# Performance work log

Measured on AMD Instinct MI355X. Metric: run time of the kernel, lower is better.

The kernel has to match this reference:

```python
import jax, jax.numpy as jnp
import numpy as np
from jax import lax

EPS = 1e-6            # cfg.positive
GAUSS_DIM = (32, 32)  # cfg.iou_gauss_dim
TOP_K_CONF = 100      # cfg.nms_top_k_conf
TOP_K_IOU = 20        # cfg.nms_top_k_iou


def unnormal_gaussian(mask_shape, loc):
    # loc: [B, N, 4] = (cx, cy, w, h) in normalized [0,1] coords.
    # Unnormalized anisotropic gaussian rendered on an HxW grid.
    H, W = mask_shape
    cx, cy, w, h = loc[..., 0], loc[..., 1], loc[..., 2], loc[..., 3]
    ys = (jnp.arange(H, dtype=loc.dtype) + 0.5) / H
    xs = (jnp.arange(W, dtype=loc.dtype) + 0.5) / W
    dx = (xs[None, None, None, :] - cx[..., None, None]) / (w[..., None, None] + 1e-4)
    dy = (ys[None, None, :, None] - cy[..., None, None]) / (h[..., None, None] + 1e-4)
    return jnp.exp(-0.5 * (dx * dx + dy * dy))  # [B, N, H, W]


def _take2(t, idx):
    # twoIndexThree: t [B,N,D], idx [B,K] -> [B,K,D]
    return jnp.take_along_axis(t, idx[..., None], axis=1)


def detect(conf, loc, mask):
    # conf: [B,P] object scores; loc: [B,P,4]; mask: [B,P,Dm]
    sorted_conf, idx = lax.top_k(conf, TOP_K_CONF)
    sorted_loc = _take2(loc, idx)
    sorted_mask = _take2(mask, idx)
    g = unnormal_gaussian(GAUSS_DIM, sorted_loc)  # [B,N,Hg,Wg]
    # pairwise gaussian IoU: sum(min) / sum(max); use min+max == a+b identity
    inter = jnp.sum(jnp.minimum(g[:, :, None], g[:, None, :]), axis=(-2, -1))  # [B,N,N]
    s = jnp.sum(g, axis=(-2, -1))
    union = s[:, :, None] + s[:, None, :] - inter
    iou = inter / union
    iou_max = jnp.max(jnp.triu(iou, 1), axis=1)   # max overlap with any earlier (higher-conf) box
    _, keep = lax.top_k(-iou_max, TOP_K_IOU)      # keep K least-overlapping boxes
    return iou, sorted_loc, sorted_mask, sorted_conf, keep


def ae_scaled_loss(original, iou, keep, loc, conf):
    conf_matrix = conf[:, :, None] * conf[:, None, :]   # outer product [B,N,N]
    final_scale = iou * jnp.triu(conf_matrix, 1)
    kept_loc = _take2(loc, keep)                        # [B,K,4]
    # surrogate AutoEncoder per-box loss (AutoEncoder class not in source)
    ae_loss = jnp.mean(kept_loc ** 2, axis=-1)          # [B,K]
    B, N = final_scale.shape[0], final_scale.shape[1]
    K = keep.shape[1]
    ae_grid = jnp.zeros_like(final_scale).at[jnp.arange(B)[:, None], keep].set(
        jnp.broadcast_to(ae_loss[..., None], (B, K, N)))
    return jnp.mean(ae_grid * final_scale)


def variance_loss(original, loc, mask, conf, proto):
    B, C, H, W = original.shape
    Hp, Wp = proto.shape[1], proto.shape[2]
    ug = unnormal_gaussian((Hp, Wp), loc)                           # [B,K,Hp,Wp]
    assembled = jax.nn.sigmoid(jnp.einsum('bhwp,bkp->bkhw', proto, mask))  # lincomb
    attention = assembled * ug
    mc = attention * conf[:, :, None, None]                         # maskConfidence
    denom = jnp.sum(mc, axis=1, keepdims=True) + EPS
    final_conf = 1.0 - jnp.sum(mc * mc / denom, axis=1)             # [B,Hp,Wp]
    final_conf = jnp.where(jnp.isnan(final_conf), 0.0, final_conf)
    # bilinear, align_corners=False == jax linear resize (half-pixel centers)
    resized = jax.image.resize(final_conf[:, None], (B, 1, H, W), method='linear')[:, 0]
    total = jnp.sum(resized, axis=0)                                 # [H,W]
    wmean = jnp.einsum('bchw,bhw->chw', original, resized) / total
    sq = (original - wmean) ** 2
    wvar = sq * resized[:, None] / (total + EPS)
    return jnp.sum(wvar) / Hp * B


def reference(original, loc, conf, mask, proto):
    conf_p = jax.nn.softmax(conf, axis=2)[:, :, 1]
    iou, s_loc, s_mask, s_conf, keep = detect(conf_p, loc, mask)
    ae = ae_scaled_loss(original, iou, keep, s_loc, s_conf)
    k_loc = _take2(s_loc, keep)
    k_mask = _take2(s_mask, keep)
    k_conf = jnp.take_along_axis(s_conf, keep, axis=1)
    var = variance_loss(original, k_loc, k_mask, k_conf, proto)
    return jnp.stack([var, ae])  # [variance_loss, ae_loss]


def setup_inputs() -> dict:
    key = jax.random.key(0)
    k1, k2, k3, k4, k5, k6 = jax.random.split(key, 6)
    B, P, Dm = 2, 19248, 32
    H = W = 550
    Hp = Wp = 138
    original = jax.random.normal(k1, (B, 3, H, W), dtype=jnp.float32)
    centers = jax.random.uniform(k2, (B, P, 2), dtype=jnp.float32)
    sizes = jax.random.uniform(k3, (B, P, 2), dtype=jnp.float32, minval=0.1, maxval=0.5)
    loc = jnp.concatenate([centers, sizes], axis=-1)                 # (cx,cy,w,h)
    conf = jax.random.normal(k4, (B, P, 2), dtype=jnp.float32)
    mask = jax.random.normal(k5, (B, P, Dm), dtype=jnp.float32) * 0.2
    proto = jax.random.normal(k6, (B, Hp, Wp, Dm), dtype=jnp.float32) * 0.5
    return {"original": original, "loc": loc, "conf": conf, "mask": mask, "proto": proto}
```

## Files before the change

kernel.cpp:

```cpp
#include <hip/hip_runtime.h>
#include <hip/hip_bf16.h>
#include <math.h>

constexpr int B   = 2;
constexpr int P   = 19248;
constexpr int N   = 100;
constexpr int K   = 20;
constexpr int GD  = 32;
constexpr int GP  = GD * GD;
constexpr int HP  = 138;
constexpr int HPP = HP * HP;
constexpr int H   = 550;
constexpr int W   = 550;
constexpr int DM  = 32;
constexpr float EPS = 1e-6f;
constexpr int NBIN = 2048;
constexpr int CAND = 2048;
constexpr int NPAIR = N * (N - 1) / 2;

constexpr int OFS_IDX   = 0;
constexpr int OFS_SCONF = OFS_IDX   + B * N;
constexpr int OFS_SLOC  = OFS_SCONF + B * N;
constexpr int OFS_IOU   = OFS_SLOC  + B * N * 4;
constexpr int OFS_KLOC  = OFS_IOU   + B * N * N;
constexpr int OFS_KMASK = OFS_KLOC  + B * K * 4;
constexpr int OFS_KCONF = OFS_KMASK + B * K * DM;
constexpr int OFS_FC    = OFS_KCONF + B * K;

__global__ __launch_bounds__(1024) void k_topk(
    const float* __restrict__ conf, const float* __restrict__ loc,
    float* __restrict__ wsf, int* __restrict__ wsi, float* __restrict__ out) {
  const int b = blockIdx.x;
  const int t = threadIdx.x;
  constexpr int EPT = (P + 1023) / 1024;
  if (b == 0 && t < 2) out[t] = 0.0f;

  __shared__ int   hist[NBIN];
  __shared__ int   s_T, s_cnt;
  __shared__ float cv[CAND];
  __shared__ int   ci[CAND];
  __shared__ float outv[N];
  __shared__ int   outi[N];

  for (int q = t; q < NBIN; q += 1024) hist[q] = 0;
  if (t == 0) s_cnt = 0;
  __syncthreads();

  float v[EPT];
#pragma unroll
  for (int j = 0; j < EPT; j++) {
    int p = j * 1024 + t;
    if (p < P) {
      float c0 = conf[(b * P + p) * 2 + 0];
      float c1 = conf[(b * P + p) * 2 + 1];
      float m  = fmaxf(c0, c1);
      float e0 = expf(c0 - m), e1 = expf(c1 - m);
      v[j] = e1 / (e0 + e1);
      atomicAdd(&hist[__float_as_uint(v[j]) >> 19], 1);
    } else {
      v[j] = -1.0f;
    }
  }
  __syncthreads();

  if (t == 0) {
    int acc = 0, bin = NBIN - 1;
    for (; bin >= 0; bin--) { acc += hist[bin]; if (acc >= N) break; }
    s_T = bin;
  }
  __syncthreads();
  const int T = s_T;

#pragma unroll
  for (int j = 0; j < EPT; j++) {
    int p = j * 1024 + t;
    if (p < P && (int)(__float_as_uint(v[j]) >> 19) >= T) {
      int pos = atomicAdd(&s_cnt, 1);
      if (pos < CAND) { cv[pos] = v[j]; ci[pos] = p; }
    }
  }
  __syncthreads();
  const int M = min(s_cnt, CAND);

#pragma unroll
  for (int q = 0; q < CAND / 1024; q++) {
    int c = t + q * 1024;
    if (c < M) {
      float mv = cv[c]; int mi = ci[c];
      int rank = 0;
      for (int j = 0; j < M; j++) {
        float jv = cv[j]; int ji = ci[j];
        rank += (jv > mv || (jv == mv && ji < mi)) ? 1 : 0;
      }
      if (rank < N) { outv[rank] = mv; outi[rank] = mi; }
    }
  }
  __syncthreads();

  if (t < N) {
    wsi[OFS_IDX + b * N + t]   = outi[t];
    wsf[OFS_SCONF + b * N + t] = outv[t];
  }
  if (t < N * 4) {
    int k = t >> 2, d = t & 3;
    wsf[OFS_SLOC + (b * N + k) * 4 + d] = loc[(b * P + outi[k]) * 4 + d];
  }
}

__global__ __launch_bounds__(256) void k_iou(float* __restrict__ wsf) {
  const int blk = blockIdx.x;
  const int b = blk / NPAIR;
  const int r = blk - b * NPAIR;
  int i = (int)((199.0f - sqrtf((float)(39601 - 8 * r))) * 0.5f);
  i = min(max(i, 0), N - 2);
  while (i < N - 2 && ((i + 1) * (2 * N - 2 - i)) / 2 <= r) i++;
  while (i > 0 && (i * (2 * N - 1 - i)) / 2 > r) i--;
  const int j = i + 1 + (r - (i * (2 * N - 1 - i)) / 2);

  const int t = threadIdx.x;
  const float* li = &wsf[OFS_SLOC + (b * N + i) * 4];
  const float* lj = &wsf[OFS_SLOC + (b * N + j) * 4];
  const float cxi = li[0], cyi = li[1], wi = li[2], hi = li[3];
  const float cxj = lj[0], cyj = lj[1], wj = lj[2], hj = lj[3];

  float smin = 0.0f, ssi = 0.0f, ssj = 0.0f;
#pragma unroll
  for (int q = 0; q < 4; q++) {
    int pix = t + q * 256;
    int y = pix >> 5, x = pix & 31;
    float xs = (x + 0.5f) / 32.0f, ys = (y + 0.5f) / 32.0f;
    float dxi = (xs - cxi) / (wi + 1e-4f);
    float dyi = (ys - cyi) / (hi + 1e-4f);
    float gi = expf(-0.5f * (dxi * dxi + dyi * dyi));
    float dxj = (xs - cxj) / (wj + 1e-4f);
    float dyj = (ys - cyj) / (hj + 1e-4f);
    float gj = expf(-0.5f * (dxj * dxj + dyj * dyj));
    smin += fminf(gi, gj);
    ssi += gi;
    ssj += gj;
  }
  for (int off = 32; off > 0; off >>= 1) {
    smin += __shfl_down(smin, off);
    ssi  += __shfl_down(ssi, off);
    ssj  += __shfl_down(ssj, off);
  }
  __shared__ float sp[3][4];
  if ((t & 63) == 0) {
    int w4 = t >> 6;
    sp[0][w4] = smin; sp[1][w4] = ssi; sp[2][w4] = ssj;
  }
  __syncthreads();
  if (t == 0) {
    float inter = sp[0][0] + sp[0][1] + sp[0][2] + sp[0][3];
    float si    = sp[1][0] + sp[1][1] + sp[1][2] + sp[1][3];
    float sj    = sp[2][0] + sp[2][1] + sp[2][2] + sp[2][3];
    wsf[OFS_IOU + (b * N + i) * N + j] = inter / (si + sj - inter);
  }
}

__global__ __launch_bounds__(1024) void k_select(
    const float* __restrict__ mask, float* __restrict__ wsf,
    int* __restrict__ wsi, float* __restrict__ out) {
  const int b = blockIdx.x;
  const int t = threadIdx.x;
  __shared__ float siou[N * N];
  __shared__ float sconf[N];
  __shared__ unsigned int mbits[N];
  __shared__ int   keep[K];
  __shared__ float coef[K];
  __shared__ float red[16];

  for (int idx = t; idx < N * N; idx += 1024) {
    int row = idx / N, col = idx - row * N;
    siou[idx] = (col > row) ? wsf[OFS_IOU + b * N * N + idx] : 0.0f;
  }
  if (t < N) { sconf[t] = wsf[OFS_SCONF + b * N + t]; mbits[t] = 0u; }
  __syncthreads();

  for (int idx = t; idx < N * N; idx += 1024) {
    int col = idx % N;
    atomicMax(&mbits[col], __float_as_uint(siou[idx]));
  }
  __syncthreads();

  if (t < N) {
    unsigned int vb = mbits[t];
    int rank = 0;
    for (int j = 0; j < N; j++) {
      unsigned int jb = mbits[j];
      rank += (jb < vb || (jb == vb && j < t)) ? 1 : 0;
    }
    if (rank < K) keep[rank] = t;
  }
  __syncthreads();

  if (t < K) {
    int r = keep[t];
    float c = sconf[r];
    wsf[OFS_KCONF + b * K + t] = c;
    const float* kl = &wsf[OFS_SLOC + (b * N + r) * 4];
    float ael = 0.25f * (kl[0] * kl[0] + kl[1] * kl[1] + kl[2] * kl[2] + kl[3] * kl[3]);
    coef[t] = ael * c;
  }
  if (t < K * 4) {
    int k = t >> 2, d = t & 3;
    wsf[OFS_KLOC + (b * K + k) * 4 + d] = wsf[OFS_SLOC + (b * N + keep[k]) * 4 + d];
  }
  if (t < K * DM) {
    int k = t >> 5, d = t & 31;
    int orig = wsi[OFS_IDX + b * N + keep[k]];
    wsf[OFS_KMASK + (b * K + k) * DM + d] = mask[(b * P + orig) * DM + d];
  }
  __syncthreads();

  float acc = 0.0f;
  for (int kc = t; kc < K * N; kc += 1024) {
    int k = kc / N, c = kc - k * N;
    int r = keep[k];
    if (c > r) acc += siou[r * N + c] * sconf[c] * coef[k];
  }
  for (int off = 32; off > 0; off >>= 1) acc += __shfl_down(acc, off);
  if ((t & 63) == 0) red[t >> 6] = acc;
  __syncthreads();
  if (t == 0) {
    float s = 0.0f;
    for (int w2 = 0; w2 < 16; w2++) s += red[w2];
    atomicAdd(out + 1, s * (1.0f / (float)(B * N * N)));
  }
}

__global__ __launch_bounds__(256) void k_fc(
    const float* __restrict__ proto, float* __restrict__ wsf) {
  const int b = blockIdx.y;
  const int t = threadIdx.x;
  const int pix = blockIdx.x * 256 + t;
  __shared__ float kl[K * 4];
  __shared__ float kc[K];
  __shared__ float km[K * DM];
  for (int q = t; q < K * 4; q += 256) kl[q] = wsf[OFS_KLOC + b * K * 4 + q];
  for (int q = t; q < K; q += 256) kc[q] = wsf[OFS_KCONF + b * K + q];
  for (int q = t; q < K * DM; q += 256) km[q] = wsf[OFS_KMASK + b * K * DM + q];
  __syncthreads();
  if (pix >= HPP) return;
  const int h = pix / HP, w2 = pix - h * HP;

  float pv[DM];
  const float4* pp = (const float4*)&proto[(size_t)(b * HPP + pix) * DM];
#pragma unroll
  for (int q = 0; q < DM / 4; q++) {
    float4 f = pp[q];
    pv[q * 4 + 0] = f.x; pv[q * 4 + 1] = f.y;
    pv[q * 4 + 2] = f.z; pv[q * 4 + 3] = f.w;
  }
  const float ysv = (h + 0.5f) / 138.0f;
  const float xsv = (w2 + 0.5f) / 138.0f;
  float sum1 = 0.0f, sum2 = 0.0f;
#pragma unroll
  for (int k = 0; k < K; k++) {
    float dot = 0.0f;
#pragma unroll
    for (int d = 0; d < DM; d++) dot += pv[d] * km[k * DM + d];
    float a  = 1.0f / (1.0f + expf(-dot));
    float dx = (xsv - kl[k * 4 + 0]) / (kl[k * 4 + 2] + 1e-4f);
    float dy = (ysv - kl[k * 4 + 1]) / (kl[k * 4 + 3] + 1e-4f);
    float ug = expf(-0.5f * (dx * dx + dy * dy));
    float att = a * ug * kc[k];
    sum1 += att;
    sum2 += att * att;
  }
  float fc = 1.0f - sum2 / (sum1 + EPS);
  if (fc != fc) fc = 0.0f;
  wsf[OFS_FC + b * HPP + pix] = fc;
}

__global__ __launch_bounds__(256) void k_var(
    const float* __restrict__ orig, const float* __restrict__ wsf,
    float* __restrict__ out) {
  const int t = threadIdx.x;
  float acc = 0.0f;
  for (int pix = blockIdx.x * 256 + t; pix < H * W; pix += 256 * 256) {
    const int h = pix / W, w2 = pix - h * W;
    const float sc = 138.0f / 550.0f;
    float sy = (h + 0.5f) * sc - 0.5f;
    float sx = (w2 + 0.5f) * sc - 0.5f;
    float fy0 = floorf(sy), fx0 = floorf(sx);
    float wy = sy - fy0, wx = sx - fx0;
    int y0 = max(0, (int)fy0), y1 = min(HP - 1, (int)fy0 + 1);
    int x0 = max(0, (int)fx0), x1 = min(HP - 1, (int)fx0 + 1);
    float r0, r1;
    {
      const float* fc = &wsf[OFS_FC + 0 * HPP];
      float v00 = fc[y0 * HP + x0], v01 = fc[y0 * HP + x1];
      float v10 = fc[y1 * HP + x0], v11 = fc[y1 * HP + x1];
      float top = v00 + (v01 - v00) * wx;
      float bot = v10 + (v11 - v10) * wx;
      r0 = top + (bot - top) * wy;
    }
    {
      const float* fc = &wsf[OFS_FC + 1 * HPP];
      float v00 = fc[y0 * HP + x0], v01 = fc[y0 * HP + x1];
      float v10 = fc[y1 * HP + x0], v11 = fc[y1 * HP + x1];
      float top = v00 + (v01 - v00) * wx;
      float bot = v10 + (v11 - v10) * wx;
      r1 = top + (bot - top) * wy;
    }
    float total = r0 + r1;
    float inv_t = 1.0f / total;
    float inv_te = 1.0f / (total + EPS);
#pragma unroll
    for (int c = 0; c < 3; c++) {
      float o0 = orig[((0 * 3 + c) * H + h) * W + w2];
      float o1 = orig[((1 * 3 + c) * H + h) * W + w2];
      float wm = (o0 * r0 + o1 * r1) * inv_t;
      float d0 = o0 - wm, d1 = o1 - wm;
      acc += (d0 * d0 * r0 + d1 * d1 * r1) * inv_te;
    }
  }
  for (int off = 32; off > 0; off >>= 1) acc += __shfl_down(acc, off);
  __shared__ float sp[4];
  if ((t & 63) == 0) sp[t >> 6] = acc;
  __syncthreads();
  if (t == 0)
    atomicAdd(out + 0, (sp[0] + sp[1] + sp[2] + sp[3]) * ((float)B / (float)HP));
}

extern "C" void kernel_launch(void* const* d_in, const int* in_sizes, int n_in,
                              void* d_out, int out_size, void* d_ws,
                              size_t ws_size, hipStream_t stream) {
  (void)in_sizes; (void)n_in; (void)out_size; (void)ws_size;
  const float* original = (const float*)d_in[0];
  const float* loc      = (const float*)d_in[1];
  const float* conf     = (const float*)d_in[2];
  const float* mask     = (const float*)d_in[3];
  const float* proto    = (const float*)d_in[4];
  float* out = (float*)d_out;
  float* wsf = (float*)d_ws;
  int*   wsi = (int*)d_ws;

  k_topk<<<B, 1024, 0, stream>>>(conf, loc, wsf, wsi, out);
  k_iou<<<B * NPAIR, 256, 0, stream>>>(wsf);
  k_select<<<B, 1024, 0, stream>>>(mask, wsf, wsi, out);
  k_fc<<<dim3((HPP + 255) / 256, B), 256, 0, stream>>>(proto, wsf);
  k_var<<<256, 256, 0, stream>>>(original, wsf, out);
}
```

Before: 134.6 us.

## Fuse all stages into one persistent kernel with software grid barriers

Merges the five kernels (top-k, pairwise IoU, keep-selection, proto attention map and variance) into one persistent 256-block kernel, separated by atomic-counter grid barriers, so launch gaps disappear. The IoU stage now uses one wavefront per pair instead of one 256-thread block per pair. The fc map is computed per output tile into shared memory and read there for the bilinear upsample, so no global fc buffer is needed. In exchange it recomputes fc at overlapping tile halos, and it depends on all 256 blocks of 1024 threads being resident at once, or the spin barriers deadlock.

```diff
diff --git a/kernel.cpp b/kernel.cpp
--- a/kernel.cpp
+++ b/kernel.cpp
@@ -6,8 +6,6 @@
 constexpr int P   = 19248;
 constexpr int N   = 100;
 constexpr int K   = 20;
-constexpr int GD  = 32;
-constexpr int GP  = GD * GD;
 constexpr int HP  = 138;
 constexpr int HPP = HP * HP;
 constexpr int H   = 550;
@@ -17,6 +15,9 @@
 constexpr int NBIN = 2048;
 constexpr int CAND = 2048;
 constexpr int NPAIR = N * (N - 1) / 2;
+constexpr int GRID = 256;
+constexpr int TS = 32;
+constexpr int TG = (W + TS - 1) / TS;
 
 constexpr int OFS_IDX   = 0;
 constexpr int OFS_SCONF = OFS_IDX   + B * N;
@@ -25,303 +26,317 @@
 constexpr int OFS_KLOC  = OFS_IOU   + B * N * N;
 constexpr int OFS_KMASK = OFS_KLOC  + B * K * 4;
 constexpr int OFS_KCONF = OFS_KMASK + B * K * DM;
-constexpr int OFS_FC    = OFS_KCONF + B * K;
-
-__global__ __launch_bounds__(1024) void k_topk(
-    const float* __restrict__ conf, const float* __restrict__ loc,
-    float* __restrict__ wsf, int* __restrict__ wsi, float* __restrict__ out) {
-  const int b = blockIdx.x;
+constexpr int OFS_BAR   = OFS_KCONF + B * K;
+
+__device__ __forceinline__ void grid_barrier(unsigned int* cnt) {
+  __syncthreads();
+  if (threadIdx.x == 0) {
+    __threadfence();
+    atomicAdd(cnt, 1u);
+    while (atomicAdd(cnt, 0u) < (unsigned)GRID) { }
+    __threadfence();
+  }
+  __syncthreads();
+}
+
+__global__ __launch_bounds__(1024) void k_fused(
+    const float* __restrict__ original, const float* __restrict__ loc,
+    const float* __restrict__ conf, const float* __restrict__ mask,
+    const float* __restrict__ proto, float* __restrict__ wsf,
+    int* __restrict__ wsi, unsigned int* __restrict__ bar,
+    float* __restrict__ out) {
+  const int blk = blockIdx.x;
   const int t = threadIdx.x;
-  constexpr int EPT = (P + 1023) / 1024;
-  if (b == 0 && t < 2) out[t] = 0.0f;
-
-  __shared__ int   hist[NBIN];
-  __shared__ int   s_T, s_cnt;
-  __shared__ float cv[CAND];
-  __shared__ int   ci[CAND];
+
+  __shared__ float smem[N * N];
   __shared__ float outv[N];
   __shared__ int   outi[N];
-
-  for (int q = t; q < NBIN; q += 1024) hist[q] = 0;
-  if (t == 0) s_cnt = 0;
-  __syncthreads();
-
-  float v[EPT];
-#pragma unroll
-  for (int j = 0; j < EPT; j++) {
-    int p = j * 1024 + t;
-    if (p < P) {
-      float c0 = conf[(b * P + p) * 2 + 0];
-      float c1 = conf[(b * P + p) * 2 + 1];
-      float m  = fmaxf(c0, c1);
-      float e0 = expf(c0 - m), e1 = expf(c1 - m);
-      v[j] = e1 / (e0 + e1);
-      atomicAdd(&hist[__float_as_uint(v[j]) >> 19], 1);
-    } else {
-      v[j] = -1.0f;
-    }
-  }
-  __syncthreads();
-
-  if (t == 0) {
-    int acc = 0, bin = NBIN - 1;
-    for (; bin >= 0; bin--) { acc += hist[bin]; if (acc >= N) break; }
-    s_T = bin;
-  }
-  __syncthreads();
-  const int T = s_T;
-
-#pragma unroll
-  for (int j = 0; j < EPT; j++) {
-    int p = j * 1024 + t;
-    if (p < P && (int)(__float_as_uint(v[j]) >> 19) >= T) {
-      int pos = atomicAdd(&s_cnt, 1);
-      if (pos < CAND) { cv[pos] = v[j]; ci[pos] = p; }
-    }
-  }
-  __syncthreads();
-  const int M = min(s_cnt, CAND);
-
-#pragma unroll
-  for (int q = 0; q < CAND / 1024; q++) {
-    int c = t + q * 1024;
-    if (c < M) {
-      float mv = cv[c]; int mi = ci[c];
-      int rank = 0;
-      for (int j = 0; j < M; j++) {
-        float jv = cv[j]; int ji = ci[j];
-        rank += (jv > mv || (jv == mv && ji < mi)) ? 1 : 0;
-      }
-      if (rank < N) { outv[rank] = mv; outi[rank] = mi; }
-    }
-  }
-  __syncthreads();
-
-  if (t < N) {
-    wsi[OFS_IDX + b * N + t]   = outi[t];
-    wsf[OFS_SCONF + b * N + t] = outv[t];
-  }
-  if (t < N * 4) {
-    int k = t >> 2, d = t & 3;
-    wsf[OFS_SLOC + (b * N + k) * 4 + d] = loc[(b * P + outi[k]) * 4 + d];
-  }
-}
-
-__global__ __launch_bounds__(256) void k_iou(float* __restrict__ wsf) {
-  const int blk = blockIdx.x;
-  const int b = blk / NPAIR;
-  const int r = blk - b * NPAIR;
-  int i = (int)((199.0f - sqrtf((float)(39601 - 8 * r))) * 0.5f);
-  i = min(max(i, 0), N - 2);
-  while (i < N - 2 && ((i + 1) * (2 * N - 2 - i)) / 2 <= r) i++;
-  while (i > 0 && (i * (2 * N - 1 - i)) / 2 > r) i--;
-  const int j = i + 1 + (r - (i * (2 * N - 1 - i)) / 2);
-
-  const int t = threadIdx.x;
-  const float* li = &wsf[OFS_SLOC + (b * N + i) * 4];
-  const float* lj = &wsf[OFS_SLOC + (b * N + j) * 4];
-  const float cxi = li[0], cyi = li[1], wi = li[2], hi = li[3];
-  const float cxj = lj[0], cyj = lj[1], wj = lj[2], hj = lj[3];
-
-  float smin = 0.0f, ssi = 0.0f, ssj = 0.0f;
-#pragma unroll
-  for (int q = 0; q < 4; q++) {
-    int pix = t + q * 256;
-    int y = pix >> 5, x = pix & 31;
-    float xs = (x + 0.5f) / 32.0f, ys = (y + 0.5f) / 32.0f;
-    float dxi = (xs - cxi) / (wi + 1e-4f);
-    float dyi = (ys - cyi) / (hi + 1e-4f);
-    float gi = expf(-0.5f * (dxi * dxi + dyi * dyi));
-    float dxj = (xs - cxj) / (wj + 1e-4f);
-    float dyj = (ys - cyj) / (hj + 1e-4f);
-    float gj = expf(-0.5f * (dxj * dxj + dyj * dyj));
-    smin += fminf(gi, gj);
-    ssi += gi;
-    ssj += gj;
-  }
-  for (int off = 32; off > 0; off >>= 1) {
-    smin += __shfl_down(smin, off);
-    ssi  += __shfl_down(ssi, off);
-    ssj  += __shfl_down(ssj, off);
-  }
-  __shared__ float sp[3][4];
-  if ((t & 63) == 0) {
-    int w4 = t >> 6;
-    sp[0][w4] = smin; sp[1][w4] = ssi; sp[2][w4] = ssj;
-  }
-  __syncthreads();
-  if (t == 0) {
-    float inter = sp[0][0] + sp[0][1] + sp[0][2] + sp[0][3];
-    float si    = sp[1][0] + sp[1][1] + sp[1][2] + sp[1][3];
-    float sj    = sp[2][0] + sp[2][1] + sp[2][2] + sp[2][3];
-    wsf[OFS_IOU + (b * N + i) * N + j] = inter / (si + sj - inter);
-  }
-}
-
-__global__ __launch_bounds__(1024) void k_select(
-    const float* __restrict__ mask, float* __restrict__ wsf,
-    int* __restrict__ wsi, float* __restrict__ out) {
-  const int b = blockIdx.x;
-  const int t = threadIdx.x;
-  __shared__ float siou[N * N];
   __shared__ float sconf[N];
   __shared__ unsigned int mbits[N];
   __shared__ int   keep[K];
   __shared__ float coef[K];
   __shared__ float red[16];
-
-  for (int idx = t; idx < N * N; idx += 1024) {
-    int row = idx / N, col = idx - row * N;
-    siou[idx] = (col > row) ? wsf[OFS_IOU + b * N * N + idx] : 0.0f;
-  }
-  if (t < N) { sconf[t] = wsf[OFS_SCONF + b * N + t]; mbits[t] = 0u; }
-  __syncthreads();
-
-  for (int idx = t; idx < N * N; idx += 1024) {
-    int col = idx % N;
-    atomicMax(&mbits[col], __float_as_uint(siou[idx]));
-  }
-  __syncthreads();
-
-  if (t < N) {
-    unsigned int vb = mbits[t];
-    int rank = 0;
-    for (int j = 0; j < N; j++) {
-      unsigned int jb = mbits[j];
-      rank += (jb < vb || (jb == vb && j < t)) ? 1 : 0;
-    }
-    if (rank < K) keep[rank] = t;
-  }
-  __syncthreads();
-
-  if (t < K) {
-    int r = keep[t];
-    float c = sconf[r];
-    wsf[OFS_KCONF + b * K + t] = c;
-    const float* kl = &wsf[OFS_SLOC + (b * N + r) * 4];
-    float ael = 0.25f * (kl[0] * kl[0] + kl[1] * kl[1] + kl[2] * kl[2] + kl[3] * kl[3]);
-    coef[t] = ael * c;
-  }
-  if (t < K * 4) {
-    int k = t >> 2, d = t & 3;
-    wsf[OFS_KLOC + (b * K + k) * 4 + d] = wsf[OFS_SLOC + (b * N + keep[k]) * 4 + d];
-  }
-  if (t < K * DM) {
-    int k = t >> 5, d = t & 31;
-    int orig = wsi[OFS_IDX + b * N + keep[k]];
-    wsf[OFS_KMASK + (b * K + k) * DM + d] = mask[(b * P + orig) * DM + d];
-  }
-  __syncthreads();
-
-  float acc = 0.0f;
-  for (int kc = t; kc < K * N; kc += 1024) {
-    int k = kc / N, c = kc - k * N;
-    int r = keep[k];
-    if (c > r) acc += siou[r * N + c] * sconf[c] * coef[k];
-  }
-  for (int off = 32; off > 0; off >>= 1) acc += __shfl_down(acc, off);
-  if ((t & 63) == 0) red[t >> 6] = acc;
-  __syncthreads();
-  if (t == 0) {
-    float s = 0.0f;
-    for (int w2 = 0; w2 < 16; w2++) s += red[w2];
-    atomicAdd(out + 1, s * (1.0f / (float)(B * N * N)));
-  }
-}
-
-__global__ __launch_bounds__(256) void k_fc(
-    const float* __restrict__ proto, float* __restrict__ wsf) {
-  const int b = blockIdx.y;
-  const int t = threadIdx.x;
-  const int pix = blockIdx.x * 256 + t;
-  __shared__ float kl[K * 4];
-  __shared__ float kc[K];
-  __shared__ float km[K * DM];
-  for (int q = t; q < K * 4; q += 256) kl[q] = wsf[OFS_KLOC + b * K * 4 + q];
-  for (int q = t; q < K; q += 256) kc[q] = wsf[OFS_KCONF + b * K + q];
-  for (int q = t; q < K * DM; q += 256) km[q] = wsf[OFS_KMASK + b * K * DM + q];
-  __syncthreads();
-  if (pix >= HPP) return;
-  const int h = pix / HP, w2 = pix - h * HP;
-
-  float pv[DM];
-  const float4* pp = (const float4*)&proto[(size_t)(b * HPP + pix) * DM];
-#pragma unroll
-  for (int q = 0; q < DM / 4; q++) {
-    float4 f = pp[q];
-    pv[q * 4 + 0] = f.x; pv[q * 4 + 1] = f.y;
-    pv[q * 4 + 2] = f.z; pv[q * 4 + 3] = f.w;
-  }
-  const float ysv = (h + 0.5f) / 138.0f;
-  const float xsv = (w2 + 0.5f) / 138.0f;
-  float sum1 = 0.0f, sum2 = 0.0f;
-#pragma unroll
-  for (int k = 0; k < K; k++) {
-    float dot = 0.0f;
-#pragma unroll
-    for (int d = 0; d < DM; d++) dot += pv[d] * km[k * DM + d];
-    float a  = 1.0f / (1.0f + expf(-dot));
-    float dx = (xsv - kl[k * 4 + 0]) / (kl[k * 4 + 2] + 1e-4f);
-    float dy = (ysv - kl[k * 4 + 1]) / (kl[k * 4 + 3] + 1e-4f);
-    float ug = expf(-0.5f * (dx * dx + dy * dy));
-    float att = a * ug * kc[k];
-    sum1 += att;
-    sum2 += att * att;
-  }
-  float fc = 1.0f - sum2 / (sum1 + EPS);
-  if (fc != fc) fc = 0.0f;
-  wsf[OFS_FC + b * HPP + pix] = fc;
-}
-
-__global__ __launch_bounds__(256) void k_var(
-    const float* __restrict__ orig, const float* __restrict__ wsf,
-    float* __restrict__ out) {
-  const int t = threadIdx.x;
-  float acc = 0.0f;
-  for (int pix = blockIdx.x * 256 + t; pix < H * W; pix += 256 * 256) {
-    const int h = pix / W, w2 = pix - h * W;
+  __shared__ int   s_T, s_cnt;
+
+  if (blk < B) {
+    const int b = blk;
+    if (b == 0 && t < 2) out[t] = 0.0f;
+    int*   hist = (int*)smem;
+    float* cv   = smem + NBIN;
+    int*   ci   = (int*)(smem + 2 * NBIN);
+    constexpr int EPT = (P + 1023) / 1024;
+
+    for (int q = t; q < NBIN; q += 1024) hist[q] = 0;
+    if (t == 0) s_cnt = 0;
+    __syncthreads();
+
+    float v[EPT];
+#pragma unroll
+    for (int j = 0; j < EPT; j++) {
+      int p = j * 1024 + t;
+      if (p < P) {
+        float c0 = conf[(b * P + p) * 2 + 0];
+        float c1 = conf[(b * P + p) * 2 + 1];
+        float m  = fmaxf(c0, c1);
+        float e0 = expf(c0 - m), e1 = expf(c1 - m);
+        v[j] = e1 / (e0 + e1);
+        atomicAdd(&hist[__float_as_uint(v[j]) >> 19], 1);
+      } else {
+        v[j] = -1.0f;
+      }
+    }
+    __syncthreads();
+
+    if (t == 0) {
+      int acc = 0, bin = NBIN - 1;
+      for (; bin >= 0; bin--) { acc += hist[bin]; if (acc >= N) break; }
+      s_T = bin;
+    }
+    __syncthreads();
+    const int T = s_T;
+
+#pragma unroll
+    for (int j = 0; j < EPT; j++) {
+      int p = j * 1024 + t;
+      if (p < P && (int)(__float_as_uint(v[j]) >> 19) >= T) {
+        int pos = atomicAdd(&s_cnt, 1);
+        if (pos < CAND) { cv[pos] = v[j]; ci[pos] = p; }
+      }
+    }
+    __syncthreads();
+    const int M = min(s_cnt, CAND);
+
+#pragma unroll
+    for (int q = 0; q < CAND / 1024; q++) {
+      int c = t + q * 1024;
+      if (c < M) {
+        float mv = cv[c]; int mi = ci[c];
+        int rank = 0;
+        for (int j = 0; j < M; j++) {
+          float jv = cv[j]; int ji = ci[j];
+          rank += (jv > mv || (jv == mv && ji < mi)) ? 1 : 0;
+        }
+        if (rank < N) { outv[rank] = mv; outi[rank] = mi; }
+      }
+    }
+    __syncthreads();
+
+    if (t < N) {
+      wsi[OFS_IDX + b * N + t]   = outi[t];
+      wsf[OFS_SCONF + b * N + t] = outv[t];
+    }
+    if (t < N * 4) {
+      int k = t >> 2, d = t & 3;
+      wsf[OFS_SLOC + (b * N + k) * 4 + d] = loc[(b * P + outi[k]) * 4 + d];
+    }
+  }
+  grid_barrier(bar + 0);
+
+  {
+    const int lane = t & 63;
+    const int wv = blk * 16 + (t >> 6);
+    for (int pr = wv; pr < B * NPAIR; pr += GRID * 16) {
+      const int b = pr / NPAIR;
+      const int r = pr - b * NPAIR;
+      int i = (int)((199.0f - sqrtf((float)(39601 - 8 * r))) * 0.5f);
+      i = min(max(i, 0), N - 2);
+      while (i < N - 2 && ((i + 1) * (2 * N - 2 - i)) / 2 <= r) i++;
+      while (i > 0 && (i * (2 * N - 1 - i)) / 2 > r) i--;
+      const int j = i + 1 + (r - (i * (2 * N - 1 - i)) / 2);
+
+      const float* li = &wsf[OFS_SLOC + (b * N + i) * 4];
+      const float* lj = &wsf[OFS_SLOC + (b * N + j) * 4];
+      const float cxi = li[0], cyi = li[1], wi = li[2], hi = li[3];
+      const float cxj = lj[0], cyj = lj[1], wj = lj[2], hj = lj[3];
+
+      float smin = 0.0f, ssi = 0.0f, ssj = 0.0f;
+#pragma unroll
+      for (int q = 0; q < 16; q++) {
+        int pix = lane + q * 64;
+        int y = pix >> 5, x = pix & 31;
+        float xs = (x + 0.5f) / 32.0f, ys = (y + 0.5f) / 32.0f;
+        float dxi = (xs - cxi) / (wi + 1e-4f);
+        float dyi = (ys - cyi) / (hi + 1e-4f);
+        float gi = expf(-0.5f * (dxi * dxi + dyi * dyi));
+        float dxj = (xs - cxj) / (wj + 1e-4f);
+        float dyj = (ys - cyj) / (hj + 1e-4f);
+        float gj = expf(-0.5f * (dxj * dxj + dyj * dyj));
+        smin += fminf(gi, gj);
+        ssi += gi;
+        ssj += gj;
+      }
+      for (int off = 32; off > 0; off >>= 1) {
+        smin += __shfl_down(smin, off);
+        ssi  += __shfl_down(ssi, off);
+        ssj  += __shfl_down(ssj, off);
+      }
+      if (lane == 0)
+        wsf[OFS_IOU + (b * N + i) * N + j] = smin / (ssi + ssj - smin);
+    }
+  }
+  grid_barrier(bar + 1);
+
+  if (blk < B) {
+    const int b = blk;
+    float* siou = smem;
+    for (int idx = t; idx < N * N; idx += 1024) {
+      int row = idx / N, col = idx - row * N;
+      siou[idx] = (col > row) ? wsf[OFS_IOU + b * N * N + idx] : 0.0f;
+    }
+    if (t < N) { sconf[t] = wsf[OFS_SCONF + b * N + t]; mbits[t] = 0u; }
+    __syncthreads();
+
+    for (int idx = t; idx < N * N; idx += 1024) {
+      int col = idx % N;
+      atomicMax(&mbits[col], __float_as_uint(siou[idx]));
+    }
+    __syncthreads();
+
+    if (t < N) {
+      unsigned int vb = mbits[t];
+      int rank = 0;
+      for (int j = 0; j < N; j++) {
+        unsigned int jb = mbits[j];
+        rank += (jb < vb || (jb == vb && j < t)) ? 1 : 0;
+      }
+      if (rank < K) keep[rank] = t;
+    }
+    __syncthreads();
+
+    if (t < K) {
+      int r = keep[t];
+      float c = sconf[r];
+      wsf[OFS_KCONF + b * K + t] = c;
+      const float* kl = &wsf[OFS_SLOC + (b * N + r) * 4];
+      float ael = 0.25f * (kl[0]*kl[0] + kl[1]*kl[1] + kl[2]*kl[2] + kl[3]*kl[3]);
+      coef[t] = ael * c;
+    }
+    if (t < K * 4) {
+      int k = t >> 2, d = t & 3;
+      wsf[OFS_KLOC + (b * K + k) * 4 + d] = wsf[OFS_SLOC + (b * N + keep[k]) * 4 + d];
+    }
+    if (t < K * DM) {
+      int k = t >> 5, d = t & 31;
+      int orig_i = wsi[OFS_IDX + b * N + keep[k]];
+      wsf[OFS_KMASK + (b * K + k) * DM + d] = mask[(b * P + orig_i) * DM + d];
+    }
+    __syncthreads();
+
+    float acc = 0.0f;
+    for (int kc = t; kc < K * N; kc += 1024) {
+      int k = kc / N, c = kc - k * N;
+      int r = keep[k];
+      if (c > r) acc += siou[r * N + c] * sconf[c] * coef[k];
+    }
+    for (int off = 32; off > 0; off >>= 1) acc += __shfl_down(acc, off);
+    if ((t & 63) == 0) red[t >> 6] = acc;
+    __syncthreads();
+    if (t == 0) {
+      float s = 0.0f;
+      for (int w2 = 0; w2 < 16; w2++) s += red[w2];
+      atomicAdd(out + 1, s * (1.0f / (float)(B * N * N)));
+    }
+  }
+  grid_barrier(bar + 2);
+
+  {
+    for (int q = t; q < B * K * 4; q += 1024) smem[q] = wsf[OFS_KLOC + q];
+    for (int q = t; q < B * K; q += 1024) smem[160 + q] = wsf[OFS_KCONF + q];
+    for (int q = t; q < B * K * DM; q += 1024) smem[200 + q] = wsf[OFS_KMASK + q];
+    float* dfc = smem + 1480;
     const float sc = 138.0f / 550.0f;
-    float sy = (h + 0.5f) * sc - 0.5f;
-    float sx = (w2 + 0.5f) * sc - 0.5f;
-    float fy0 = floorf(sy), fx0 = floorf(sx);
-    float wy = sy - fy0, wx = sx - fx0;
-    int y0 = max(0, (int)fy0), y1 = min(HP - 1, (int)fy0 + 1);
-    int x0 = max(0, (int)fx0), x1 = min(HP - 1, (int)fx0 + 1);
-    float r0, r1;
-    {
-      const float* fc = &wsf[OFS_FC + 0 * HPP];
-      float v00 = fc[y0 * HP + x0], v01 = fc[y0 * HP + x1];
-      float v10 = fc[y1 * HP + x0], v11 = fc[y1 * HP + x1];
-      float top = v00 + (v01 - v00) * wx;
-      float bot = v10 + (v11 - v10) * wx;
-      r0 = top + (bot - top) * wy;
-    }
-    {
-      const float* fc = &wsf[OFS_FC + 1 * HPP];
-      float v00 = fc[y0 * HP + x0], v01 = fc[y0 * HP + x1];
-      float v10 = fc[y1 * HP + x0], v11 = fc[y1 * HP + x1];
-      float top = v00 + (v01 - v00) * wx;
-      float bot = v10 + (v11 - v10) * wx;
-      r1 = top + (bot - top) * wy;
-    }
-    float total = r0 + r1;
-    float inv_t = 1.0f / total;
-    float inv_te = 1.0f / (total + EPS);
-#pragma unroll
-    for (int c = 0; c < 3; c++) {
-      float o0 = orig[((0 * 3 + c) * H + h) * W + w2];
-      float o1 = orig[((1 * 3 + c) * H + h) * W + w2];
-      float wm = (o0 * r0 + o1 * r1) * inv_t;
-      float d0 = o0 - wm, d1 = o1 - wm;
-      acc += (d0 * d0 * r0 + d1 * d1 * r1) * inv_te;
-    }
-  }
-  for (int off = 32; off > 0; off >>= 1) acc += __shfl_down(acc, off);
-  __shared__ float sp[4];
-  if ((t & 63) == 0) sp[t >> 6] = acc;
-  __syncthreads();
-  if (t == 0)
-    atomicAdd(out + 0, (sp[0] + sp[1] + sp[2] + sp[3]) * ((float)B / (float)HP));
+    float vacc = 0.0f;
+
+    for (int tile = blk; tile < TG * TG; tile += GRID) {
+      int ty = tile / TG, tx = tile - ty * TG;
+      int h0 = ty * TS, w0 = tx * TS;
+      int cy_base = (int)floorf((h0 + 0.5f) * sc - 0.5f);
+      int cx_base = (int)floorf((w0 + 0.5f) * sc - 0.5f);
+      __syncthreads();
+
+      if (t < B * 100) {
+        int bb = t / 100, rem = t - bb * 100;
+        int sy = rem / 10, sx = rem - sy * 10;
+        int gy = min(HP - 1, max(0, cy_base + sy));
+        int gx = min(HP - 1, max(0, cx_base + sx));
+        float pv2[DM];
+        const float4* pp = (const float4*)&proto[(size_t)(bb * HPP + gy * HP + gx) * DM];
+#pragma unroll
+        for (int q = 0; q < DM / 4; q++) {
+          float4 f = pp[q];
+          pv2[q*4+0] = f.x; pv2[q*4+1] = f.y; pv2[q*4+2] = f.z; pv2[q*4+3] = f.w;
+        }
+        const float ysv = (gy + 0.5f) / 138.0f;
+        const float xsv = (gx + 0.5f) / 138.0f;
+        float sum1 = 0.0f, sum2 = 0.0f;
+#pragma unroll
+        for (int k = 0; k < K; k++) {
+          float dot = 0.0f;
+#pragma unroll
+          for (int d = 0; d < DM; d++) dot += pv2[d] * smem[200 + (bb * K + k) * DM + d];
+          float a  = 1.0f / (1.0f + expf(-dot));
+          float dx = (xsv - smem[(bb * K + k) * 4 + 0]) / (smem[(bb * K + k) * 4 + 2] + 1e-4f);
+          float dy = (ysv - smem[(bb * K + k) * 4 + 1]) / (smem[(bb * K + k) * 4 + 3] + 1e-4f);
+          float ug = expf(-0.5f * (dx * dx + dy * dy));
+          float att = a * ug * smem[160 + bb * K + k];
+          sum1 += att;
+          sum2 += att * att;
+        }
+        float fc = 1.0f - sum2 / (sum1 + EPS);
+        if (fc != fc) fc = 0.0f;
+        dfc[t] = fc;
+      }
+      __syncthreads();
+
+      int h = h0 + (t >> 5), w2 = w0 + (t & 31);
+      if (h < H && w2 < W) {
+        float sy = (h + 0.5f) * sc - 0.5f;
+        float sx = (w2 + 0.5f) * sc - 0.5f;
+        float fy0 = floorf(sy), fx0 = floorf(sx);
+        float wy = sy - fy0, wx = sx - fx0;
+        int iy0 = (int)fy0 - cy_base;
+        int ix0 = (int)fx0 - cx_base;
+        float r0, r1;
+        {
+          const float* fc = dfc;
+          float v00 = fc[iy0*10+ix0], v01 = fc[iy0*10+ix0+1];
+          float v10 = fc[(iy0+1)*10+ix0], v11 = fc[(iy0+1)*10+ix0+1];
+          float top = v00 + (v01 - v00) * wx;
+          float bot = v10 + (v11 - v10) * wx;
+          r0 = top + (bot - top) * wy;
+        }
+        {
+          const float* fc = dfc + 100;
+          float v00 = fc[iy0*10+ix0], v01 = fc[iy0*10+ix0+1];
+          float v10 = fc[(iy0+1)*10+ix0], v11 = fc[(iy0+1)*10+ix0+1];
+          float top = v00 + (v01 - v00) * wx;
+          float bot = v10 + (v11 - v10) * wx;
+          r1 = top + (bot - top) * wy;
+        }
+        float total = r0 + r1;
+        float inv_t = 1.0f / total;
+        float inv_te = 1.0f / (total + EPS);
+#pragma unroll
+        for (int c = 0; c < 3; c++) {
+          float o0 = original[((0 * 3 + c) * H + h) * W + w2];
+          float o1 = original[((1 * 3 + c) * H + h) * W + w2];
+          float wm = (o0 * r0 + o1 * r1) * inv_t;
+          float d0 = o0 - wm, d1 = o1 - wm;
+          vacc += (d0 * d0 * r0 + d1 * d1 * r1) * inv_te;
+        }
+      }
+    }
+
+    for (int off = 32; off > 0; off >>= 1) vacc += __shfl_down(vacc, off);
+    __syncthreads();
+    if ((t & 63) == 0) red[t >> 6] = vacc;
+    __syncthreads();
+    if (t == 0) {
+      float s = 0.0f;
+      for (int w2 = 0; w2 < 16; w2++) s += red[w2];
+      if (s != 0.0f) atomicAdd(out + 0, s * ((float)B / (float)HP));
+    }
+  }
 }
 
 extern "C" void kernel_launch(void* const* d_in, const int* in_sizes, int n_in,
@@ -336,10 +351,9 @@
   float* out = (float*)d_out;
   float* wsf = (float*)d_ws;
   int*   wsi = (int*)d_ws;
-
-  k_topk<<<B, 1024, 0, stream>>>(conf, loc, wsf, wsi, out);
-  k_iou<<<B * NPAIR, 256, 0, stream>>>(wsf);
-  k_select<<<B, 1024, 0, stream>>>(mask, wsf, wsi, out);
-  k_fc<<<dim3((HPP + 255) / 256, B), 256, 0, stream>>>(proto, wsf);
-  k_var<<<256, 256, 0, stream>>>(original, wsf, out);
+  unsigned int* bar = (unsigned int*)(wsi + OFS_BAR);
+
+  hipMemsetAsync(bar, 0, 3 * sizeof(unsigned int), stream);
+  k_fused<<<GRID, 1024, 0, stream>>>(original, loc, conf, mask, proto,
+                                     wsf, wsi, bar, out);
 }
```

Result: slower. 179.8 us (+33.6%).
